# Kernel tuning notes

Hardware: AMD Instinct MI355X
Metric: run time of the kernel (lower is better)

## Reference

```python
import jax, jax.numpy as jnp
import numpy as np

N_UNI = 32; N_G = 4; N_PPG = 8
MAX_D = 100.0; MIN_D = 0.5
SOM_SIGMA = 2.0; G_STD = 2.5
ORIG = jnp.array([-25.6, -25.6, -2.0], jnp.float32); VS = 0.4
NZ = 16; GW = 128; GL = 128; DIM = 128
H_IMG = 352; W_IMG = 1216

def pe(x):
    # positional encoding: num_freqs=6, include_input -> 3 + 36 = 39 dims
    f = 2.0 ** jnp.arange(6, dtype=x.dtype)
    xf = x[..., None] * f  # (...,3,6)
    s = x.shape[:-1]
    return jnp.concatenate([x, jnp.sin(xf).reshape(s + (18,)), jnp.cos(xf).reshape(s + (18,))], axis=-1)

def resnet_fc(z, x, P):
    # pixelNeRF-style ResnetFC with latent injection per block
    w_in, b_in, wz, bz, w0, b0, w1, b1, w_out, b_out = P
    h = x @ w_in + b_in
    for i in range(3):
        h = h + z @ wz[i] + bz[i]
        net = jax.nn.relu(h) @ w0[i] + b0[i]
        h = h + jax.nn.relu(net) @ w1[i] + b1[i]
    return jax.nn.relu(h) @ w_out + b_out

def trilinear(grid, pts):
    # grid: (NZ,GW,GL,DIM); pts: (N,3) lidar coords -> trilinear gather, 0 outside
    g = (pts - ORIG) / VS
    gx, gy, gz = g[:, 0], g[:, 1], g[:, 2]
    inb = (gx >= 0) & (gx <= GW - 1) & (gy >= 0) & (gy <= GL - 1) & (gz >= 0) & (gz <= NZ - 1)
    gx = jnp.clip(gx, 0.0, GW - 1.0); gy = jnp.clip(gy, 0.0, GL - 1.0); gz = jnp.clip(gz, 0.0, NZ - 1.0)
    x0 = jnp.clip(jnp.floor(gx).astype(jnp.int32), 0, GW - 2)
    y0 = jnp.clip(jnp.floor(gy).astype(jnp.int32), 0, GL - 2)
    z0 = jnp.clip(jnp.floor(gz).astype(jnp.int32), 0, NZ - 2)
    fx = gx - x0; fy = gy - y0; fz = gz - z0
    def c(zi, xi, yi, w):
        return grid[zi, xi, yi] * w[:, None]
    feat = (c(z0, x0, y0, (1 - fz) * (1 - fx) * (1 - fy)) + c(z0, x0, y0 + 1, (1 - fz) * (1 - fx) * fy)
            + c(z0, x0 + 1, y0, (1 - fz) * fx * (1 - fy)) + c(z0, x0 + 1, y0 + 1, (1 - fz) * fx * fy)
            + c(z0 + 1, x0, y0, fz * (1 - fx) * (1 - fy)) + c(z0 + 1, x0, y0 + 1, fz * (1 - fx) * fy)
            + c(z0 + 1, x0 + 1, y0, fz * fx * (1 - fy)) + c(z0 + 1, x0 + 1, y0 + 1, fz * fx * fy))
    return feat * inb[:, None].astype(feat.dtype)

def bilinear(img, uv):
    # img: (3,H,W); uv: (N,2) (u=col, v=row) -> (N,3)
    _, H, W = img.shape
    u = jnp.clip(uv[:, 0], 0.0, W - 1.0); v = jnp.clip(uv[:, 1], 0.0, H - 1.0)
    u0 = jnp.clip(jnp.floor(u).astype(jnp.int32), 0, W - 2)
    v0 = jnp.clip(jnp.floor(v).astype(jnp.int32), 0, H - 2)
    fu = u - u0; fv = v - v0
    g = lambda vi, ui: img[:, vi, ui]
    out = (g(v0, u0) * ((1 - fv) * (1 - fu)) + g(v0, u0 + 1) * ((1 - fv) * fu)
           + g(v0 + 1, u0) * (fv * (1 - fu)) + g(v0 + 1, u0 + 1) * (fv * fu))
    return out.T

def _forward(bev_feature, cam_K, img_source, img_target, T_source2infer, T_source2target,
             gaussian_noise, Pm, Pg, sampled_pixels):
    R = sampled_pixels.shape[0]
    # (B, C, W, L) -> (n_z, W, L, dim)
    vf = bev_feature[0].reshape(NZ, DIM, GW, GL).transpose(0, 2, 3, 1)
    inv_K = jnp.linalg.inv(cam_K)
    pix = sampled_pixels.astype(jnp.float32)
    homog = jnp.concatenate([pix, jnp.ones((R, 1), jnp.float32)], axis=1)
    dirs = homog @ inv_K.T
    unit = dirs / jnp.linalg.norm(dirs, axis=1, keepdims=True)  # (R,3) cam frame
    Rsi = T_source2infer[:3, :3]; tsi = T_source2infer[:3, 3]
    viewdir = unit @ Rsi.T  # lidar frame

    # --- predict per-ray gaussian means/stds at coarse segment centers ---
    base = (jnp.arange(N_G, dtype=jnp.float32) + 0.5) * (MAX_D / N_G)
    pg = (unit[:, None, :] * base[None, :, None]).reshape(-1, 3) @ Rsi.T + tsi
    fg = trilinear(vf, pg)
    vdg = jnp.broadcast_to(viewdir[:, None, :], (R, N_G, 3)).reshape(-1, 3)
    og = resnet_fc(fg, jnp.concatenate([pe(pg), vdg], axis=1), Pg)  # (R*N_G,2)
    means = jnp.clip(base[None, :] + og[:, 0].reshape(R, N_G), MIN_D, MAX_D)
    stds = G_STD * jax.nn.sigmoid(og[:, 1].reshape(R, N_G)) + 0.1

    # --- sample points: uniform + gaussian, sorted along ray ---
    d_g = jnp.clip(means[:, :, None] + stds[:, :, None] * gaussian_noise, MIN_D, MAX_D).reshape(R, N_G * N_PPG)
    d_u = jnp.broadcast_to(jnp.linspace(MIN_D, MAX_D, N_UNI, dtype=jnp.float32)[None, :], (R, N_UNI))
    d = jnp.sort(jnp.concatenate([d_u, d_g], axis=1), axis=1)  # (R,64)
    P = d.shape[1]
    pl = (unit[:, None, :] * d[..., None]).reshape(-1, 3) @ Rsi.T + tsi
    fl = trilinear(vf, pl)
    vd = jnp.broadcast_to(viewdir[:, None, :], (R, P, 3)).reshape(-1, 3)
    out = resnet_fc(fl, jnp.concatenate([pe(pl), vd], axis=1), Pm).reshape(R, P, 4)
    sigma = jax.nn.softplus(out[..., 0]); rgb = jax.nn.sigmoid(out[..., 1:])

    # --- volume rendering ---
    deltas = jnp.concatenate([d[:, 1:] - d[:, :-1], jnp.full((R, 1), 1e10, jnp.float32)], axis=1)
    alpha = 1.0 - jnp.exp(-sigma * deltas)
    trans = jnp.cumprod(1.0 - alpha + 1e-10, axis=1)
    trans = jnp.concatenate([jnp.ones((R, 1), jnp.float32), trans[:, :-1]], axis=1)
    w = alpha * trans
    depth = (w * d).sum(axis=1)          # (R,)
    color = (w[..., None] * rgb).sum(axis=1)  # (R,3)

    # --- losses ---
    diff = jnp.abs(means - jax.lax.stop_gradient(depth)[:, None])
    loss_dist = diff.min(axis=1)
    pdf = jnp.exp(-(d[:, None, :] - means[..., None]) ** 2 / (2.0 * stds[..., None] ** 2)) / (stds[..., None] * jnp.sqrt(2.0 * jnp.pi))
    loss_kl = (w * (-jnp.log(pdf.mean(axis=1) + 1e-6))).sum(axis=1)
    src = bilinear(img_source, pix)
    loss_color = jnp.abs(src - color)
    pcam = unit * depth[:, None]
    pt = pcam @ T_source2target[:3, :3].T + T_source2target[:3, 3]
    proj = pt @ cam_K.T
    uv = proj[:, :2] / jnp.clip(proj[:, 2:3], 1e-3)
    tgt = bilinear(img_target, uv)
    loss_reproj = jnp.abs(src - tgt)
    total = loss_reproj.mean() + loss_color.mean() + loss_kl.mean() + 0.01 * loss_dist.mean()
    return total

def setup_inputs() -> dict:
    key = jax.random.key(0)
    def rn(i, shape, s=1.0):
        return jax.random.normal(jax.random.fold_in(key, i), shape, jnp.float32) * s
    R = 4096
    inp = {}
    inp['bev_feature'] = rn(0, (1, NZ * DIM, GW, GL), 0.5)
    inp['cam_K'] = jnp.array([[720.0, 0.0, 608.0], [0.0, 720.0, 176.0], [0.0, 0.0, 1.0]], jnp.float32)
    inp['img_source'] = jax.random.uniform(jax.random.fold_in(key, 1), (3, H_IMG, W_IMG), jnp.float32)
    inp['img_target'] = jax.random.uniform(jax.random.fold_in(key, 2), (3, H_IMG, W_IMG), jnp.float32)
    Rcl = jnp.array([[0.0, 0.0, 1.0], [-1.0, 0.0, 0.0], [0.0, -1.0, 0.0]], jnp.float32)  # cam->lidar axes
    inp['T_source2infer'] = jnp.eye(4, dtype=jnp.float32).at[:3, :3].set(Rcl).at[:3, 3].set(jnp.array([0.5, 0.2, 0.1], jnp.float32))
    inp['T_source2target'] = jnp.eye(4, dtype=jnp.float32).at[0, 3].set(0.8).at[1, 3].set(0.05)
    inp['gaussian_noise'] = rn(3, (R, N_G, N_PPG))
    u = jax.random.randint(jax.random.fold_in(key, 4), (R,), 0, W_IMG)
    v = jax.random.randint(jax.random.fold_in(key, 5), (R,), 0, H_IMG)
    inp['sampled_pixels'] = jnp.stack([u, v], axis=1).astype(jnp.int32)
    for pfx, (i0, d_out) in {'m': (10, 4), 'g': (40, 2)}.items():
        inp[pfx + '_w_in'] = rn(i0, (42, 128), 0.05)
        inp[pfx + '_b_in'] = jnp.zeros((128,), jnp.float32)
        inp[pfx + '_wz'] = rn(i0 + 1, (3, 128, 128), 0.05)
        inp[pfx + '_bz'] = jnp.zeros((3, 128), jnp.float32)
        inp[pfx + '_w0'] = rn(i0 + 2, (3, 128, 128), 0.05)
        inp[pfx + '_b0'] = jnp.zeros((3, 128), jnp.float32)
        inp[pfx + '_w1'] = rn(i0 + 3, (3, 128, 128), 0.05)
        inp[pfx + '_b1'] = jnp.zeros((3, 128), jnp.float32)
        inp[pfx + '_w_out'] = rn(i0 + 4, (128, d_out), 0.05)
        inp[pfx + '_b_out'] = jnp.zeros((d_out,), jnp.float32)
    return inp

def reference(bev_feature, cam_K, img_source, img_target, T_source2infer, T_source2target,
              gaussian_noise, sampled_pixels,
              m_w_in, m_b_in, m_wz, m_bz, m_w0, m_b0, m_w1, m_b1, m_w_out, m_b_out,
              g_w_in, g_b_in, g_wz, g_bz, g_w0, g_b0, g_w1, g_b1, g_w_out, g_b_out):
    Pm = (m_w_in, m_b_in, m_wz, m_bz, m_w0, m_b0, m_w1, m_b1, m_w_out, m_b_out)
    Pg = (g_w_in, g_b_in, g_wz, g_bz, g_w0, g_b0, g_w1, g_b1, g_w_out, g_b_out)
    return _forward(bev_feature, cam_K, img_source, img_target, T_source2infer, T_source2target,
                    gaussian_noise, Pm, Pg, sampled_pixels)
```

## Files before the change

### kernel.cpp

```cpp
#include <hip/hip_runtime.h>

typedef __attribute__((ext_vector_type(8))) short short8;
typedef __attribute__((ext_vector_type(4))) float f32x4;
typedef unsigned short ushort_t;

#define WIMG 1216
#define HIMG 352

__device__ __forceinline__ float sigmoid_(float x){ return 1.f/(1.f+__expf(-x)); }
__device__ __forceinline__ float softplus_(float x){
  return fmaxf(x,0.f) + log1pf(__expf(-fabsf(x)));
}
__device__ __forceinline__ ushort_t f2b(float x){
  union { float f; unsigned u; } v; v.f = x;
  unsigned r = v.u + 0x7FFF + ((v.u >> 16) & 1);
  return (ushort_t)(r >> 16);
}
__device__ __forceinline__ ushort_t f2b_fast(float x){
  union { float f; unsigned u; } v; v.f = x;
  return (ushort_t)((v.u + 0x8000u) >> 16);
}
__device__ __forceinline__ unsigned pack_trunc(float a, float b){
  union { float f; unsigned u; } va, vb; va.f = a; vb.f = b;
  return (va.u >> 16) | (vb.u & 0xFFFF0000u);
}
__device__ __forceinline__ float b2f_lo(unsigned u){
  union { unsigned u; float f; } v; v.u = u << 16; return v.f;
}
__device__ __forceinline__ float b2f_hi(unsigned u){
  union { unsigned u; float f; } v; v.u = u & 0xFFFF0000u; return v.f;
}

__global__ void k_pack(const float* __restrict__ w_in, const float* __restrict__ wz,
                       const float* __restrict__ w0, const float* __restrict__ w1,
                       const float* __restrict__ w_out, int outd,
                       ushort_t* __restrict__ pk){
  int id = blockIdx.x*256 + threadIdx.x;
  if (id >= 39*4096) return;
  int blk = id >> 12;
  int e = id & 4095;
  float val = 0.f;
  if (blk < 38) {
    int nt = e >> 9, lane = (e >> 3) & 63, j = e & 7;
    int kloc = (lane >> 4)*8 + j;
    int n = nt*16 + (lane & 15);
    if (blk < 2) {
      int k = blk*32 + kloc;
      val = (k < 42) ? w_in[k*128 + n] : 0.f;
    } else {
      int g = blk - 2;
      int i = g / 12, r = g % 12, m = r >> 2, ks = r & 3;
      int k = ks*32 + kloc;
      const float* src = (m==0 ? wz : (m==1 ? w0 : w1)) + i*16384;
      val = src[k*128 + n];
    }
  } else if (e < 2048) {
    int ks = e >> 9, lane = (e >> 3) & 63, j = e & 7;
    int k = ks*32 + (lane >> 4)*8 + j;
    int n = lane & 15;
    val = (n < outd) ? w_out[k*outd + n] : 0.f;
  }
  pk[id] = f2b(val);
}

__global__ void k_transpose(const float* __restrict__ src, ushort_t* __restrict__ dst){
  __shared__ float tile[32][33];
  int zx = blockIdx.z;
  int y0 = blockIdx.x * 32;
  int c0 = blockIdx.y * 32;
  int z = zx >> 7, x = zx & 127;
  const float* s = src + (size_t)z*2097152 + (size_t)x*128;
  for (int i = threadIdx.y; i < 32; i += 8)
    tile[i][threadIdx.x] = __builtin_nontemporal_load(s + (size_t)(c0+i)*16384 + (size_t)(y0 + threadIdx.x));
  __syncthreads();
  ushort_t* d = dst + ((size_t)zx*128 + y0)*128 + c0;
  int idx = threadIdx.y*32 + threadIdx.x;
  for (int it = 0; it < 2; ++it) {
    int lin = it*256 + idx;
    int y = lin >> 4, cp = lin & 15;
    unsigned o = pack_trunc(tile[cp*2][y], tile[cp*2+1][y]);
    __builtin_nontemporal_store(o, (unsigned*)(d + (size_t)y*128 + cp*2));
  }
}

__global__ void k_rayinit(const float* __restrict__ camK, const int* __restrict__ pix,
                          const float* __restrict__ Tsi,
                          float* __restrict__ unit, float* __restrict__ viewdir, int R){
  int r = blockIdx.x*blockDim.x + threadIdx.x;
  if (r >= R) return;
  float a=camK[0],b=camK[1],c=camK[2],d=camK[3],e=camK[4],f=camK[5],g=camK[6],h=camK[7],i=camK[8];
  float c00 = e*i-f*h, c01 = c*h-b*i, c02 = b*f-c*e;
  float c10 = f*g-d*i, c11 = a*i-c*g, c12 = c*d-a*f;
  float c20 = d*h-e*g, c21 = b*g-a*h, c22 = a*e-b*d;
  float det = a*c00 + b*c10 + c*c20;
  float id = 1.f/det;
  float u = (float)pix[2*r], v = (float)pix[2*r+1];
  float dx = (c00*u + c01*v + c02)*id;
  float dy = (c10*u + c11*v + c12)*id;
  float dz = (c20*u + c21*v + c22)*id;
  float n = sqrtf(dx*dx+dy*dy+dz*dz);
  dx/=n; dy/=n; dz/=n;
  unit[3*r]=dx; unit[3*r+1]=dy; unit[3*r+2]=dz;
  viewdir[3*r]   = Tsi[0]*dx + Tsi[1]*dy + Tsi[2]*dz;
  viewdir[3*r+1] = Tsi[4]*dx + Tsi[5]*dy + Tsi[6]*dz;
  viewdir[3*r+2] = Tsi[8]*dx + Tsi[9]*dy + Tsi[10]*dz;
}

template<int KS>
__device__ __forceinline__ void gemm_accT(const ushort_t* lds, int pitch,
                                          const ushort_t* __restrict__ pkW,
                                          f32x4 acc[2][4], int wave, int lane)
{
  int l15 = lane & 15, quad = lane >> 4;
  short8 w[KS][2];
  #pragma unroll
  for (int ks = 0; ks < KS; ++ks)
    #pragma unroll
    for (int ct = 0; ct < 2; ++ct)
      w[ks][ct] = *(const short8*)(pkW + (size_t)((ks*8 + wave*2 + ct)*64 + lane)*8);
  #pragma unroll
  for (int ks = 0; ks < KS; ++ks) {
    short8 b[4];
    #pragma unroll
    for (int nt = 0; nt < 4; ++nt)
      b[nt] = *(const short8*)(lds + (nt*16 + l15)*pitch + ks*32 + quad*8);
    #pragma unroll
    for (int ct = 0; ct < 2; ++ct)
      #pragma unroll
      for (int nt = 0; nt < 4; ++nt)
        acc[ct][nt] = __builtin_amdgcn_mfma_f32_16x16x32_bf16(w[ks][ct], b[nt], acc[ct][nt], 0,0,0);
  }
}

__device__ __forceinline__ void store_reluT(ushort_t* buf, const f32x4 acc[2][4], int wave, int lane){
  int l15 = lane & 15, quad = lane >> 4;
  #pragma unroll
  for (int ct = 0; ct < 2; ++ct)
    #pragma unroll
    for (int nt = 0; nt < 4; ++nt) {
      float r0 = fmaxf(acc[ct][nt][0], 0.f);
      float r1 = fmaxf(acc[ct][nt][1], 0.f);
      float r2 = fmaxf(acc[ct][nt][2], 0.f);
      float r3 = fmaxf(acc[ct][nt][3], 0.f);
      uint2 o; o.x = pack_trunc(r0, r1); o.y = pack_trunc(r2, r3);
      *(uint2*)(buf + (nt*16 + l15)*136 + (wave*2+ct)*16 + quad*4) = o;
    }
}

template<int OUTD, int RAY_SHIFT>
__global__ __launch_bounds__(256, 4)
void k_fused(const ushort_t* __restrict__ vfh, const float* __restrict__ vf0, int mode,
             const float* __restrict__ unit, const float* __restrict__ viewdir,
             const float* __restrict__ Tsi, const float* __restrict__ dvals,
             const ushort_t* __restrict__ pk,
             const float* __restrict__ b_in, const float* __restrict__ bzv,
             const float* __restrict__ b0v, const float* __restrict__ b1v,
             const float* __restrict__ b_out,
             float* __restrict__ means, float* __restrict__ stds, float* __restrict__ outbuf)
{
  __shared__ int   sOff[64];
  __shared__ float sW[64][8];
  __shared__ float sPx[64], sPy[64], sPz[64], sVx[64], sVy[64], sVz[64];
  __shared__ ushort_t zf[64*136];
  __shared__ ushort_t Wb[64*136];

  int tid = threadIdx.x;
  int qbase = blockIdx.x * 64;

  if (tid < 64) {
    int q = qbase + tid;
    int ray = q >> RAY_SHIFT;
    float t;
    if constexpr (OUTD == 2) t = ((float)(q & 3) + 0.5f) * 25.f;
    else                     t = dvals[q];
    float ux = unit[3*ray], uy = unit[3*ray+1], uz = unit[3*ray+2];
    float wx=ux*t, wy=uy*t, wz=uz*t;
    float px = Tsi[0]*wx + Tsi[1]*wy + Tsi[2]*wz + Tsi[3];
    float py = Tsi[4]*wx + Tsi[5]*wy + Tsi[6]*wz + Tsi[7];
    float pz = Tsi[8]*wx + Tsi[9]*wy + Tsi[10]*wz + Tsi[11];
    sPx[tid]=px; sPy[tid]=py; sPz[tid]=pz;
    sVx[tid]=viewdir[3*ray]; sVy[tid]=viewdir[3*ray+1]; sVz[tid]=viewdir[3*ray+2];
    float gx = (px + 25.6f)*2.5f;
    float gy = (py + 25.6f)*2.5f;
    float gz = (pz + 2.0f)*2.5f;
    bool inb = (gx>=0.f)&&(gx<=127.f)&&(gy>=0.f)&&(gy<=127.f)&&(gz>=0.f)&&(gz<=15.f);
    gx = fminf(fmaxf(gx,0.f),127.f);
    gy = fminf(fmaxf(gy,0.f),127.f);
    gz = fminf(fmaxf(gz,0.f),15.f);
    int x0 = min(max((int)floorf(gx),0),126);
    int y0 = min(max((int)floorf(gy),0),126);
    int z0 = min(max((int)floorf(gz),0),14);
    float fx = gx-(float)x0, fy = gy-(float)y0, fz = gz-(float)z0;
    float sc = inb ? 1.f : 0.f;
    float ax0 = 1.f-fx, ay0 = 1.f-fy;
    float az0 = (1.f-fz)*sc, az1 = fz*sc;
    float q00 = ax0*ay0, q01 = ax0*fy, q10 = fx*ay0, q11 = fx*fy;
    sW[tid][0] = az0*q00; sW[tid][1] = az0*q01; sW[tid][2] = az0*q10; sW[tid][3] = az0*q11;
    sW[tid][4] = az1*q00; sW[tid][5] = az1*q01; sW[tid][6] = az1*q10; sW[tid][7] = az1*q11;
    sOff[tid] = mode ? (((z0*128 + x0)*128 + y0)*128)
                     : (z0*2097152 + x0*128 + y0);
  }
  __syncthreads();

  for (int it = 0; it < 4; ++it) {
    int lin = it*256 + tid;
    int p = lin >> 4, cb = lin & 15;
    float4 wA = *(const float4*)&sW[p][0];
    float4 wB = *(const float4*)&sW[p][4];
    float r0=0,r1=0,r2=0,r3=0,r4=0,r5=0,r6=0,r7=0;
    if (mode) {
      const ushort_t* b = vfh + sOff[p] + cb*8;
      uint4 v;
      #define ACC8(PTR, W) \
        v = *(const uint4*)(PTR); \
        r0 += (W)*b2f_lo(v.x); r1 += (W)*b2f_hi(v.x); \
        r2 += (W)*b2f_lo(v.y); r3 += (W)*b2f_hi(v.y); \
        r4 += (W)*b2f_lo(v.z); r5 += (W)*b2f_hi(v.z); \
        r6 += (W)*b2f_lo(v.w); r7 += (W)*b2f_hi(v.w);
      ACC8(b,                     wA.x)
      ACC8(b + 128,               wA.y)
      ACC8(b + 16384,             wA.z)
      ACC8(b + 16384 + 128,       wA.w)
      ACC8(b + 2097152,           wB.x)
      ACC8(b + 2097152 + 128,     wB.y)
      ACC8(b + 2097152 + 16384,   wB.z)
      ACC8(b + 2097152 + 16512,   wB.w)
      #undef ACC8
    } else {
      const float* bsrc = vf0 + sOff[p];
      float rr[8];
      #pragma unroll
      for (int k = 0; k < 8; ++k) {
        const float* bc = bsrc + (size_t)(cb*8 + k)*16384;
        rr[k] = wA.x*bc[0] + wA.y*bc[1] + wA.z*bc[128] + wA.w*bc[129]
              + wB.x*bc[2097152] + wB.y*bc[2097153] + wB.z*bc[2097280] + wB.w*bc[2097281];
      }
      r0=rr[0]; r1=rr[1]; r2=rr[2]; r3=rr[3]; r4=rr[4]; r5=rr[5]; r6=rr[6]; r7=rr[7];
    }
    uint4 o;
    o.x = pack_trunc(r0, r1); o.y = pack_trunc(r2, r3);
    o.z = pack_trunc(r4, r5); o.w = pack_trunc(r6, r7);
    *(uint4*)(zf + p*136 + cb*8) = o;
  }

  for (int it = 0; it < 16; ++it) {
    int lin = it*256 + tid;
    int p = lin >> 6, d = lin & 63;
    float val = 0.f;
    if (d < 3)      val = (d==0)?sPx[p]:((d==1)?sPy[p]:sPz[p]);
    else if (d < 39) {
      int s = d - 3; bool isSin = (s < 18); if (!isSin) s -= 18;
      int axis = s/6, fi = s%6;
      float base = (axis==0)?sPx[p]:((axis==1)?sPy[p]:sPz[p]);
      float arg = base * (float)(1 << fi);
      val = isSin ? __sinf(arg) : __cosf(arg);
    } else if (d < 42) {
      val = (d==39)?sVx[p]:((d==40)?sVy[p]:sVz[p]);
    }
    Wb[p*72 + d] = f2b_fast(val);
  }
  __syncthreads();

  int wave = tid >> 6, lane = tid & 63;
  int l15 = lane & 15, quad = lane >> 4;
  int cbase = wave*32 + quad*4;

  f32x4 h[2][4];
  {
    f32x4 bi0 = *(const f32x4*)(b_in + cbase);
    f32x4 bi1 = *(const f32x4*)(b_in + cbase + 16);
    #pragma unroll
    for (int nt = 0; nt < 4; ++nt) { h[0][nt] = bi0; h[1][nt] = bi1; }
  }
  gemm_accT<2>(Wb, 72, pk, h, wave, lane);

  const ushort_t* pkl = pk + 2*4096;
  #pragma unroll 1
  for (int i = 0; i < 3; ++i) {
    gemm_accT<4>(zf, 136, pkl + (size_t)(i*12)*4096, h, wave, lane);
    {
      f32x4 bz0 = *(const f32x4*)(bzv + i*128 + cbase);
      f32x4 bz1 = *(const f32x4*)(bzv + i*128 + cbase + 16);
      #pragma unroll
      for (int nt = 0; nt < 4; ++nt) { h[0][nt] += bz0; h[1][nt] += bz1; }
    }
    __syncthreads();
    store_reluT(Wb, h, wave, lane);
    __syncthreads();
    f32x4 net[2][4];
    {
      f32x4 c0b = *(const f32x4*)(b0v + i*128 + cbase);
      f32x4 c1b = *(const f32x4*)(b0v + i*128 + cbase + 16);
      #pragma unroll
      for (int nt = 0; nt < 4; ++nt) { net[0][nt] = c0b; net[1][nt] = c1b; }
    }
    gemm_accT<4>(Wb, 136, pkl + (size_t)(i*12+4)*4096, net, wave, lane);
    __syncthreads();
    store_reluT(Wb, net, wave, lane);
    __syncthreads();
    gemm_accT<4>(Wb, 136, pkl + (size_t)(i*12+8)*4096, h, wave, lane);
    {
      f32x4 o0b = *(const f32x4*)(b1v + i*128 + cbase);
      f32x4 o1b = *(const f32x4*)(b1v + i*128 + cbase + 16);
      #pragma unroll
      for (int nt = 0; nt < 4; ++nt) { h[0][nt] += o0b; h[1][nt] += o1b; }
    }
  }
  __syncthreads();
  store_reluT(Wb, h, wave, lane);
  __syncthreads();

  {
    const ushort_t* pkw = pk + 38*4096;
    f32x4 oa = (f32x4){0.f,0.f,0.f,0.f};
    #pragma unroll
    for (int ks = 0; ks < 4; ++ks) {
      short8 w = *(const short8*)(pkw + (size_t)(ks*64 + lane)*8);
      short8 b = *(const short8*)(Wb + (wave*16 + l15)*136 + ks*32 + quad*8);
      oa = __builtin_amdgcn_mfma_f32_16x16x32_bf16(w, b, oa, 0,0,0);
    }
    if (quad == 0) {
      int q = qbase + wave*16 + l15;
      if constexpr (OUTD == 4) {
        float4 o = { oa[0] + b_out[0], oa[1] + b_out[1], oa[2] + b_out[2], oa[3] + b_out[3] };
        *(float4*)(outbuf + (size_t)q*4) = o;
      } else {
        int g = q & 3;
        means[q] = fminf(fmaxf(((float)g + 0.5f)*25.f + oa[0] + b_out[0], 0.5f), 100.f);
        stds[q]  = 2.5f*sigmoid_(oa[1] + b_out[1]) + 0.1f;
      }
    }
  }
}

__global__ void k_sortd(const float* __restrict__ means, const float* __restrict__ stds,
                        const float* __restrict__ noise, float* __restrict__ dsort, int R){
  __shared__ float buf[4][64];
  int lr = threadIdx.x >> 6, p = threadIdx.x & 63;
  int ray = blockIdx.x*4 + lr;
  float val;
  if (p < 32) val = 0.5f + (float)p * (99.5f/31.f);
  else {
    int idx = p - 32, g = idx >> 3, s = idx & 7;
    float mu = means[ray*4+g], sd = stds[ray*4+g];
    val = fminf(fmaxf(mu + sd*noise[(ray*4+g)*8 + s], 0.5f), 100.f);
  }
  buf[lr][p] = val;
  __syncthreads();
  int rank = 0;
  for (int k = 0; k < 64; ++k) {
    float o = buf[lr][k];
    rank += (o < val) || (o == val && k < p);
  }
  dsort[ray*64 + rank] = val;
}

__device__ __forceinline__ void bilin3(const float* __restrict__ img, float u, float v, float* out){
  u = fminf(fmaxf(u, 0.f), (float)(WIMG-1));
  v = fminf(fmaxf(v, 0.f), (float)(HIMG-1));
  int u0 = min(max((int)floorf(u),0), WIMG-2);
  int v0 = min(max((int)floorf(v),0), HIMG-2);
  float fu = u - (float)u0, fv = v - (float)v0;
  float w00=(1.f-fv)*(1.f-fu), w01=(1.f-fv)*fu, w10=fv*(1.f-fu), w11=fv*fu;
  #pragma unroll
  for (int c = 0; c < 3; ++c) {
    const float* b = img + (size_t)c*(HIMG*WIMG) + (size_t)v0*WIMG + u0;
    out[c] = w00*b[0] + w01*b[1] + w10*b[WIMG] + w11*b[WIMG+1];
  }
}

__global__ void k_render(const float* __restrict__ outbuf, const float* __restrict__ dsort,
                         const float* __restrict__ means, const float* __restrict__ stds,
                         const float* __restrict__ unit,
                         const float* __restrict__ img_src, const float* __restrict__ img_tgt,
                         const int* __restrict__ pix, const float* __restrict__ camK,
                         const float* __restrict__ Tst, float* __restrict__ rayloss, int R){
  int gid = blockIdx.x*blockDim.x + threadIdx.x;
  int r = gid >> 6, lane = gid & 63;
  if (r >= R) return;
  float d = dsort[(size_t)r*64 + lane];
  float dn = __shfl_down(d, 1);
  float delta = (lane < 63) ? (dn - d) : 1e10f;
  float4 o = *(const float4*)(outbuf + (size_t)r*256 + lane*4);
  float sig = softplus_(o.x);
  float alpha = 1.f - __expf(-sig*delta);
  float om = 1.f - alpha + 1e-10f;
  float prod = om;
  #pragma unroll
  for (int off = 1; off < 64; off <<= 1) {
    float v = __shfl_up(prod, off);
    if (lane >= off) prod *= v;
  }
  float texc = __shfl_up(prod, 1);
  if (lane == 0) texc = 1.f;
  float w = alpha * texc;
  float m0=means[r*4],m1=means[r*4+1],m2=means[r*4+2],m3=means[r*4+3];
  float s0=stds[r*4], s1=stds[r*4+1], s2=stds[r*4+2], s3=stds[r*4+3];
  float t0=(d-m0)/s0, t1=(d-m1)/s1, t2=(d-m2)/s2, t3=(d-m3)/s3;
  float pm = 0.25f*0.3989422804014327f*(__expf(-0.5f*t0*t0)/s0 + __expf(-0.5f*t1*t1)/s1
                                      + __expf(-0.5f*t2*t2)/s2 + __expf(-0.5f*t3*t3)/s3);
  float kl  = w * (-__logf(pm + 1e-6f));
  float dep = w * d;
  float c0 = w * sigmoid_(o.y);
  float c1 = w * sigmoid_(o.z);
  float c2 = w * sigmoid_(o.w);
  #pragma unroll
  for (int off = 32; off; off >>= 1) {
    dep += __shfl_xor(dep, off);
    c0  += __shfl_xor(c0, off);
    c1  += __shfl_xor(c1, off);
    c2  += __shfl_xor(c2, off);
    kl  += __shfl_xor(kl, off);
  }
  if (lane == 0) {
    float ld = fminf(fminf(fabsf(m0-dep),fabsf(m1-dep)), fminf(fabsf(m2-dep),fabsf(m3-dep)));
    float src[3], tgt[3];
    float u = (float)pix[2*r], v = (float)pix[2*r+1];
    bilin3(img_src, u, v, src);
    float ux=unit[3*r],uy=unit[3*r+1],uz=unit[3*r+2];
    float pcx=ux*dep, pcy=uy*dep, pcz=uz*dep;
    float ptx = Tst[0]*pcx + Tst[1]*pcy + Tst[2]*pcz + Tst[3];
    float pty = Tst[4]*pcx + Tst[5]*pcy + Tst[6]*pcz + Tst[7];
    float ptz = Tst[8]*pcx + Tst[9]*pcy + Tst[10]*pcz + Tst[11];
    float prx = camK[0]*ptx + camK[1]*pty + camK[2]*ptz;
    float pry = camK[3]*ptx + camK[4]*pty + camK[5]*ptz;
    float prz = camK[6]*ptx + camK[7]*pty + camK[8]*ptz;
    prz = fmaxf(prz, 0.001f);
    bilin3(img_tgt, prx/prz, pry/prz, tgt);
    float lrepr = fabsf(src[0]-tgt[0])+fabsf(src[1]-tgt[1])+fabsf(src[2]-tgt[2]);
    float lcol  = fabsf(src[0]-c0)+fabsf(src[1]-c1)+fabsf(src[2]-c2);
    float invR = 1.f/(float)R;
    rayloss[r] = (lrepr + lcol) * (invR/3.f) + kl*invR + 0.01f*ld*invR;
  }
}

__global__ void k_reduce(const float* __restrict__ rayloss, float* __restrict__ out, int R){
  __shared__ float sm[256];
  float acc = 0.f;
  for (int i = threadIdx.x; i < R; i += 256) acc += rayloss[i];
  sm[threadIdx.x] = acc;
  __syncthreads();
  for (int s = 128; s > 0; s >>= 1) {
    if ((int)threadIdx.x < s) sm[threadIdx.x] += sm[threadIdx.x + s];
    __syncthreads();
  }
  if (threadIdx.x == 0) out[0] = sm[0];
}

extern "C" void kernel_launch(void* const* d_in, const int* in_sizes, int n_in,
                              void* d_out, int out_size, void* d_ws, size_t ws_size,
                              hipStream_t stream)
{
  const float* bev   = (const float*)d_in[0];
  const float* camK  = (const float*)d_in[1];
  const float* img_s = (const float*)d_in[2];
  const float* img_t = (const float*)d_in[3];
  const float* Tsi   = (const float*)d_in[4];
  const float* Tst   = (const float*)d_in[5];
  const float* noise = (const float*)d_in[6];
  const int*   pix   = (const int*)d_in[7];
  const float* m_w_in=(const float*)d_in[8];  const float* m_b_in=(const float*)d_in[9];
  const float* m_wz  =(const float*)d_in[10]; const float* m_bz  =(const float*)d_in[11];
  const float* m_w0  =(const float*)d_in[12]; const float* m_b0  =(const float*)d_in[13];
  const float* m_w1  =(const float*)d_in[14]; const float* m_b1  =(const float*)d_in[15];
  const float* m_wo  =(const float*)d_in[16]; const float* m_bo  =(const float*)d_in[17];
  const float* g_w_in=(const float*)d_in[18]; const float* g_b_in=(const float*)d_in[19];
  const float* g_wz  =(const float*)d_in[20]; const float* g_bz  =(const float*)d_in[21];
  const float* g_w0  =(const float*)d_in[22]; const float* g_b0  =(const float*)d_in[23];
  const float* g_w1  =(const float*)d_in[24]; const float* g_b1  =(const float*)d_in[25];
  const float* g_wo  =(const float*)d_in[26]; const float* g_bo  =(const float*)d_in[27];

  int R = in_sizes[7] / 2;
  float* ws = (float*)d_ws;
  size_t off = 0;
  float* unitb = ws + off; off += (size_t)R*3;
  float* vdirb = ws + off; off += (size_t)R*3;
  float* means = ws + off; off += (size_t)R*4;
  float* stds  = ws + off; off += (size_t)R*4;
  float* dsort = ws + off; off += (size_t)R*64;
  float* outbf = ws + off; off += (size_t)R*256;
  float* rlos  = ws + off; off += (size_t)R;
  ushort_t* pkM = (ushort_t*)(ws + off);
  ushort_t* pkG = pkM + 39*4096;
  off += 39*4096 + 64;
  off = (off + 63) & ~(size_t)63;
  ushort_t* vfh = (ushort_t*)(ws + off);
  size_t need = off*4ull + (size_t)16*128*128*128*2ull;
  int mode = (ws_size >= need) ? 1 : 0;

  k_pack<<<624,256,0,stream>>>(m_w_in, m_wz, m_w0, m_w1, m_wo, 4, pkM);
  k_pack<<<624,256,0,stream>>>(g_w_in, g_wz, g_w0, g_w1, g_wo, 2, pkG);
  if (mode) {
    dim3 g(4,4,2048), b(32,8);
    k_transpose<<<g,b,0,stream>>>(bev, vfh);
  }
  k_rayinit<<<(R+255)/256,256,0,stream>>>(camK,pix,Tsi,unitb,vdirb,R);
  k_fused<2,2><<<R/16,256,0,stream>>>(vfh,bev,mode,unitb,vdirb,Tsi,nullptr,pkG,
      g_b_in,g_bz,g_b0,g_b1,g_bo, means,stds,nullptr);
  k_sortd<<<R/4,256,0,stream>>>(means,stds,noise,dsort,R);
  k_fused<4,6><<<R,256,0,stream>>>(vfh,bev,mode,unitb,vdirb,Tsi,dsort,pkM,
      m_b_in,m_bz,m_b0,m_b1,m_bo, nullptr,nullptr,outbf);
  k_render<<<R/4,256,0,stream>>>(outbf,dsort,means,stds,unitb,img_s,img_t,pix,camK,Tst,rlos,R);
  k_reduce<<<1,256,0,stream>>>(rlos,(float*)d_out,R);
}
```

Measured before the change: 458.8 us.

## Fuse ray init, depth sort and loss reduction into neighbouring kernels; retile MLP fragments

Ray-direction setup moves into the guide-MLP kernel, and the per-ray depth sampling and sort move into its epilogue. The final loss reduction becomes a per-block atomicAdd in the render kernel, and the output is zeroed inside the pack kernel. Together these remove three launches and their intermediate buffers. The MLP GEMM switches to a pre-swizzled fragment LDS layout with a 2x2 wave split, and the BEV transpose uses 64x64 tiles with vectorized loads and stores. The atomic accumulation makes the loss sum order nondeterministic.

```diff
diff --git a/kernel.cpp b/kernel.cpp
--- a/kernel.cpp
+++ b/kernel.cpp
@@ -2,6 +2,7 @@
 
 typedef __attribute__((ext_vector_type(8))) short short8;
 typedef __attribute__((ext_vector_type(4))) float f32x4;
+typedef __attribute__((ext_vector_type(2))) unsigned u32x2;
 typedef unsigned short ushort_t;
 
 #define WIMG 1216
@@ -34,7 +35,8 @@
 __global__ void k_pack(const float* __restrict__ w_in, const float* __restrict__ wz,
                        const float* __restrict__ w0, const float* __restrict__ w1,
                        const float* __restrict__ w_out, int outd,
-                       ushort_t* __restrict__ pk){
+                       ushort_t* __restrict__ pk, float* __restrict__ out0){
+  if (out0 && blockIdx.x == 0 && threadIdx.x == 0) out0[0] = 0.f;
   int id = blockIdx.x*256 + threadIdx.x;
   if (id >= 39*4096) return;
   int blk = id >> 12;
@@ -63,95 +65,79 @@
   pk[id] = f2b(val);
 }
 
-__global__ void k_transpose(const float* __restrict__ src, ushort_t* __restrict__ dst){
-  __shared__ float tile[32][33];
+__global__ __launch_bounds__(256) void k_transpose(const float* __restrict__ src, ushort_t* __restrict__ dst){
+  __shared__ float tile[64][65];
   int zx = blockIdx.z;
-  int y0 = blockIdx.x * 32;
-  int c0 = blockIdx.y * 32;
+  int y0 = blockIdx.x * 64;
+  int c0 = blockIdx.y * 64;
   int z = zx >> 7, x = zx & 127;
-  const float* s = src + (size_t)z*2097152 + (size_t)x*128;
-  for (int i = threadIdx.y; i < 32; i += 8)
-    tile[i][threadIdx.x] = __builtin_nontemporal_load(s + (size_t)(c0+i)*16384 + (size_t)(y0 + threadIdx.x));
+  const float* s = src + (size_t)z*2097152 + (size_t)c0*16384 + (size_t)x*128 + y0;
+  int tid = threadIdx.x;
+  int r0 = tid >> 4, f4 = tid & 15;
+  #pragma unroll
+  for (int it = 0; it < 4; ++it) {
+    int c = it*16 + r0;
+    f32x4 v = __builtin_nontemporal_load((const f32x4*)(s + (size_t)c*16384 + f4*4));
+    tile[c][f4*4+0]=v.x; tile[c][f4*4+1]=v.y; tile[c][f4*4+2]=v.z; tile[c][f4*4+3]=v.w;
+  }
   __syncthreads();
   ushort_t* d = dst + ((size_t)zx*128 + y0)*128 + c0;
-  int idx = threadIdx.y*32 + threadIdx.x;
-  for (int it = 0; it < 2; ++it) {
-    int lin = it*256 + idx;
-    int y = lin >> 4, cp = lin & 15;
-    unsigned o = pack_trunc(tile[cp*2][y], tile[cp*2+1][y]);
-    __builtin_nontemporal_store(o, (unsigned*)(d + (size_t)y*128 + cp*2));
-  }
-}
-
-__global__ void k_rayinit(const float* __restrict__ camK, const int* __restrict__ pix,
-                          const float* __restrict__ Tsi,
-                          float* __restrict__ unit, float* __restrict__ viewdir, int R){
-  int r = blockIdx.x*blockDim.x + threadIdx.x;
-  if (r >= R) return;
-  float a=camK[0],b=camK[1],c=camK[2],d=camK[3],e=camK[4],f=camK[5],g=camK[6],h=camK[7],i=camK[8];
-  float c00 = e*i-f*h, c01 = c*h-b*i, c02 = b*f-c*e;
-  float c10 = f*g-d*i, c11 = a*i-c*g, c12 = c*d-a*f;
-  float c20 = d*h-e*g, c21 = b*g-a*h, c22 = a*e-b*d;
-  float det = a*c00 + b*c10 + c*c20;
-  float id = 1.f/det;
-  float u = (float)pix[2*r], v = (float)pix[2*r+1];
-  float dx = (c00*u + c01*v + c02)*id;
-  float dy = (c10*u + c11*v + c12)*id;
-  float dz = (c20*u + c21*v + c22)*id;
-  float n = sqrtf(dx*dx+dy*dy+dz*dz);
-  dx/=n; dy/=n; dz/=n;
-  unit[3*r]=dx; unit[3*r+1]=dy; unit[3*r+2]=dz;
-  viewdir[3*r]   = Tsi[0]*dx + Tsi[1]*dy + Tsi[2]*dz;
-  viewdir[3*r+1] = Tsi[4]*dx + Tsi[5]*dy + Tsi[6]*dz;
-  viewdir[3*r+2] = Tsi[8]*dx + Tsi[9]*dy + Tsi[10]*dz;
+  #pragma unroll
+  for (int it = 0; it < 4; ++it) {
+    int y = it*16 + r0;
+    float a0 = tile[f4*4+0][y], a1 = tile[f4*4+1][y];
+    float a2 = tile[f4*4+2][y], a3 = tile[f4*4+3][y];
+    u32x2 o; o.x = pack_trunc(a0,a1); o.y = pack_trunc(a2,a3);
+    __builtin_nontemporal_store(o, (u32x2*)(d + (size_t)y*128 + f4*4));
+  }
 }
 
 template<int KS>
-__device__ __forceinline__ void gemm_accT(const ushort_t* lds, int pitch,
+__device__ __forceinline__ void gemm_frag(const ushort_t* lds,
                                           const ushort_t* __restrict__ pkW,
-                                          f32x4 acc[2][4], int wave, int lane)
+                                          f32x4 acc[4][2], int chalf, int phalf, int lane)
 {
+  #pragma unroll
+  for (int ks = 0; ks < KS; ++ks) {
+    short8 b[2];
+    #pragma unroll
+    for (int ntL = 0; ntL < 2; ++ntL)
+      b[ntL] = *(const short8*)(lds + (ks*4 + phalf*2 + ntL)*512 + lane*8);
+    #pragma unroll
+    for (int i = 0; i < 4; ++i) {
+      short8 w = *(const short8*)(pkW + (size_t)((ks*8 + chalf*4 + i)*64 + lane)*8);
+      #pragma unroll
+      for (int ntL = 0; ntL < 2; ++ntL)
+        acc[i][ntL] = __builtin_amdgcn_mfma_f32_16x16x32_bf16(w, b[ntL], acc[i][ntL], 0,0,0);
+    }
+  }
+}
+
+__device__ __forceinline__ void store_reluF(ushort_t* buf, const f32x4 acc[4][2],
+                                            int chalf, int phalf, int lane){
   int l15 = lane & 15, quad = lane >> 4;
-  short8 w[KS][2];
-  #pragma unroll
-  for (int ks = 0; ks < KS; ++ks)
-    #pragma unroll
-    for (int ct = 0; ct < 2; ++ct)
-      w[ks][ct] = *(const short8*)(pkW + (size_t)((ks*8 + wave*2 + ct)*64 + lane)*8);
-  #pragma unroll
-  for (int ks = 0; ks < KS; ++ks) {
-    short8 b[4];
-    #pragma unroll
-    for (int nt = 0; nt < 4; ++nt)
-      b[nt] = *(const short8*)(lds + (nt*16 + l15)*pitch + ks*32 + quad*8);
-    #pragma unroll
-    for (int ct = 0; ct < 2; ++ct)
-      #pragma unroll
-      for (int nt = 0; nt < 4; ++nt)
-        acc[ct][nt] = __builtin_amdgcn_mfma_f32_16x16x32_bf16(w[ks][ct], b[nt], acc[ct][nt], 0,0,0);
-  }
-}
-
-__device__ __forceinline__ void store_reluT(ushort_t* buf, const f32x4 acc[2][4], int wave, int lane){
-  int l15 = lane & 15, quad = lane >> 4;
-  #pragma unroll
-  for (int ct = 0; ct < 2; ++ct)
-    #pragma unroll
-    for (int nt = 0; nt < 4; ++nt) {
-      float r0 = fmaxf(acc[ct][nt][0], 0.f);
-      float r1 = fmaxf(acc[ct][nt][1], 0.f);
-      float r2 = fmaxf(acc[ct][nt][2], 0.f);
-      float r3 = fmaxf(acc[ct][nt][3], 0.f);
-      uint2 o; o.x = pack_trunc(r0, r1); o.y = pack_trunc(r2, r3);
-      *(uint2*)(buf + (nt*16 + l15)*136 + (wave*2+ct)*16 + quad*4) = o;
-    }
-}
-
-template<int OUTD, int RAY_SHIFT>
+  #pragma unroll
+  for (int i = 0; i < 4; ++i) {
+    int c = chalf*64 + i*16 + quad*4;
+    int ksp = c >> 5, k3 = (c >> 3) & 3, jj = c & 7;
+    #pragma unroll
+    for (int ntL = 0; ntL < 2; ++ntL) {
+      int nt = phalf*2 + ntL;
+      uint2 o;
+      o.x = pack_trunc(fmaxf(acc[i][ntL][0],0.f), fmaxf(acc[i][ntL][1],0.f));
+      o.y = pack_trunc(fmaxf(acc[i][ntL][2],0.f), fmaxf(acc[i][ntL][3],0.f));
+      *(uint2*)(buf + (ksp*4 + nt)*512 + (k3*16 + l15)*8 + jj) = o;
+    }
+  }
+}
+
+template<int OUTD>
 __global__ __launch_bounds__(256, 4)
 void k_fused(const ushort_t* __restrict__ vfh, const float* __restrict__ vf0, int mode,
-             const float* __restrict__ unit, const float* __restrict__ viewdir,
-             const float* __restrict__ Tsi, const float* __restrict__ dvals,
+             const float* __restrict__ camK, const int* __restrict__ pix,
+             const float* __restrict__ noise,
+             float* __restrict__ unit, float* __restrict__ viewdir,
+             const float* __restrict__ Tsi, float* __restrict__ dsort,
              const ushort_t* __restrict__ pk,
              const float* __restrict__ b_in, const float* __restrict__ bzv,
              const float* __restrict__ b0v, const float* __restrict__ b1v,
@@ -160,26 +146,62 @@
 {
   __shared__ int   sOff[64];
   __shared__ float sW[64][8];
-  __shared__ float sPx[64], sPy[64], sPz[64], sVx[64], sVy[64], sVz[64];
-  __shared__ ushort_t zf[64*136];
-  __shared__ ushort_t Wb[64*136];
+  __shared__ float sPx[64], sPy[64], sPz[64];
+  __shared__ float sUx[16], sUy[16], sUz[16], sVx[16], sVy[16], sVz[16];
+  __shared__ float sMean[64], sStd[64];
+  __shared__ __align__(16) ushort_t zf[16*512];
+  __shared__ __align__(16) ushort_t Wb[16*512];
 
   int tid = threadIdx.x;
   int qbase = blockIdx.x * 64;
 
+  if constexpr (OUTD == 2) {
+    if (tid < 16) {
+      int gray = (qbase >> 2) + tid;
+      float a=camK[0],b=camK[1],c=camK[2],d=camK[3],e=camK[4],f=camK[5],g=camK[6],h=camK[7],i=camK[8];
+      float c00 = e*i-f*h, c01 = c*h-b*i, c02 = b*f-c*e;
+      float c10 = f*g-d*i, c11 = a*i-c*g, c12 = c*d-a*f;
+      float c20 = d*h-e*g, c21 = b*g-a*h, c22 = a*e-b*d;
+      float det = a*c00 + b*c10 + c*c20;
+      float id = 1.f/det;
+      float u = (float)pix[2*gray], v = (float)pix[2*gray+1];
+      float dx = (c00*u + c01*v + c02)*id;
+      float dy = (c10*u + c11*v + c12)*id;
+      float dz = (c20*u + c21*v + c22)*id;
+      float n = sqrtf(dx*dx+dy*dy+dz*dz);
+      dx/=n; dy/=n; dz/=n;
+      sUx[tid]=dx; sUy[tid]=dy; sUz[tid]=dz;
+      unit[3*gray]=dx; unit[3*gray+1]=dy; unit[3*gray+2]=dz;
+      float vx = Tsi[0]*dx + Tsi[1]*dy + Tsi[2]*dz;
+      float vy = Tsi[4]*dx + Tsi[5]*dy + Tsi[6]*dz;
+      float vz = Tsi[8]*dx + Tsi[9]*dy + Tsi[10]*dz;
+      sVx[tid]=vx; sVy[tid]=vy; sVz[tid]=vz;
+      viewdir[3*gray]=vx; viewdir[3*gray+1]=vy; viewdir[3*gray+2]=vz;
+    }
+  } else {
+    if (tid == 0) {
+      int ray = blockIdx.x;
+      sUx[0]=unit[3*ray]; sUy[0]=unit[3*ray+1]; sUz[0]=unit[3*ray+2];
+      sVx[0]=viewdir[3*ray]; sVy[0]=viewdir[3*ray+1]; sVz[0]=viewdir[3*ray+2];
+    }
+  }
+  __syncthreads();
+
   if (tid < 64) {
-    int q = qbase + tid;
-    int ray = q >> RAY_SHIFT;
-    float t;
-    if constexpr (OUTD == 2) t = ((float)(q & 3) + 0.5f) * 25.f;
-    else                     t = dvals[q];
-    float ux = unit[3*ray], uy = unit[3*ray+1], uz = unit[3*ray+2];
+    float t, ux, uy, uz;
+    if constexpr (OUTD == 2) {
+      t = ((float)(tid & 3) + 0.5f) * 25.f;
+      int lr = tid >> 2;
+      ux = sUx[lr]; uy = sUy[lr]; uz = sUz[lr];
+    } else {
+      t = dsort[qbase + tid];
+      ux = sUx[0]; uy = sUy[0]; uz = sUz[0];
+    }
     float wx=ux*t, wy=uy*t, wz=uz*t;
     float px = Tsi[0]*wx + Tsi[1]*wy + Tsi[2]*wz + Tsi[3];
     float py = Tsi[4]*wx + Tsi[5]*wy + Tsi[6]*wz + Tsi[7];
     float pz = Tsi[8]*wx + Tsi[9]*wy + Tsi[10]*wz + Tsi[11];
     sPx[tid]=px; sPy[tid]=py; sPz[tid]=pz;
-    sVx[tid]=viewdir[3*ray]; sVy[tid]=viewdir[3*ray+1]; sVz[tid]=viewdir[3*ray+2];
     float gx = (px + 25.6f)*2.5f;
     float gy = (py + 25.6f)*2.5f;
     float gz = (pz + 2.0f)*2.5f;
@@ -240,74 +262,80 @@
     uint4 o;
     o.x = pack_trunc(r0, r1); o.y = pack_trunc(r2, r3);
     o.z = pack_trunc(r4, r5); o.w = pack_trunc(r6, r7);
-    *(uint4*)(zf + p*136 + cb*8) = o;
-  }
-
-  for (int it = 0; it < 16; ++it) {
-    int lin = it*256 + tid;
-    int p = lin >> 6, d = lin & 63;
-    float val = 0.f;
-    if (d < 3)      val = (d==0)?sPx[p]:((d==1)?sPy[p]:sPz[p]);
-    else if (d < 39) {
-      int s = d - 3; bool isSin = (s < 18); if (!isSin) s -= 18;
-      int axis = s/6, fi = s%6;
-      float base = (axis==0)?sPx[p]:((axis==1)?sPy[p]:sPz[p]);
-      float arg = base * (float)(1 << fi);
-      val = isSin ? __sinf(arg) : __cosf(arg);
-    } else if (d < 42) {
-      val = (d==39)?sVx[p]:((d==40)?sVy[p]:sVz[p]);
-    }
-    Wb[p*72 + d] = f2b_fast(val);
+    int T = (cb >> 2)*4 + (p >> 4);
+    int lanep = (cb & 3)*16 + (p & 15);
+    *(uint4*)(zf + T*512 + lanep*8) = o;
+  }
+
+  {
+    int p = tid & 63, dg = tid >> 6;
+    float px = sPx[p], py = sPy[p], pz = sPz[p];
+    int lr = (OUTD == 2) ? (p >> 2) : 0;
+    float vx = sVx[lr], vy = sVy[lr], vz = sVz[lr];
+    #pragma unroll 1
+    for (int it = 0; it < 16; ++it) {
+      int d = it*4 + dg;
+      float val = 0.f;
+      if (d < 3)      val = (d==0)?px:((d==1)?py:pz);
+      else if (d < 39) {
+        int s = d - 3; bool isSin = (s < 18); if (!isSin) s -= 18;
+        int axis = s/6, fi = s%6;
+        float base = (axis==0)?px:((axis==1)?py:pz);
+        float arg = base * (float)(1 << fi);
+        val = isSin ? __sinf(arg) : __cosf(arg);
+      } else if (d < 42) {
+        val = (d==39)?vx:((d==40)?vy:vz);
+      }
+      int addr = (d>>5)*2048 + (p>>4)*512 + (((d>>3)&3)*16 + (p&15))*8 + (d&7);
+      Wb[addr] = f2b_fast(val);
+    }
   }
   __syncthreads();
 
   int wave = tid >> 6, lane = tid & 63;
   int l15 = lane & 15, quad = lane >> 4;
-  int cbase = wave*32 + quad*4;
-
-  f32x4 h[2][4];
-  {
-    f32x4 bi0 = *(const f32x4*)(b_in + cbase);
-    f32x4 bi1 = *(const f32x4*)(b_in + cbase + 16);
-    #pragma unroll
-    for (int nt = 0; nt < 4; ++nt) { h[0][nt] = bi0; h[1][nt] = bi1; }
-  }
-  gemm_accT<2>(Wb, 72, pk, h, wave, lane);
+  int chalf = wave >> 1, phalf = wave & 1;
+  int cbase = chalf*64 + quad*4;
+
+  f32x4 h[4][2];
+  #pragma unroll
+  for (int i = 0; i < 4; ++i) {
+    f32x4 bi = *(const f32x4*)(b_in + cbase + i*16);
+    h[i][0] = bi; h[i][1] = bi;
+  }
+  gemm_frag<2>(Wb, pk, h, chalf, phalf, lane);
 
   const ushort_t* pkl = pk + 2*4096;
   #pragma unroll 1
-  for (int i = 0; i < 3; ++i) {
-    gemm_accT<4>(zf, 136, pkl + (size_t)(i*12)*4096, h, wave, lane);
-    {
-      f32x4 bz0 = *(const f32x4*)(bzv + i*128 + cbase);
-      f32x4 bz1 = *(const f32x4*)(bzv + i*128 + cbase + 16);
-      #pragma unroll
-      for (int nt = 0; nt < 4; ++nt) { h[0][nt] += bz0; h[1][nt] += bz1; }
+  for (int i3 = 0; i3 < 3; ++i3) {
+    gemm_frag<4>(zf, pkl + (size_t)(i3*12)*4096, h, chalf, phalf, lane);
+    #pragma unroll
+    for (int i = 0; i < 4; ++i) {
+      f32x4 bz = *(const f32x4*)(bzv + i3*128 + cbase + i*16);
+      h[i][0] += bz; h[i][1] += bz;
     }
     __syncthreads();
-    store_reluT(Wb, h, wave, lane);
+    store_reluF(Wb, h, chalf, phalf, lane);
     __syncthreads();
-    f32x4 net[2][4];
-    {
-      f32x4 c0b = *(const f32x4*)(b0v + i*128 + cbase);
-      f32x4 c1b = *(const f32x4*)(b0v + i*128 + cbase + 16);
-      #pragma unroll
-      for (int nt = 0; nt < 4; ++nt) { net[0][nt] = c0b; net[1][nt] = c1b; }
-    }
-    gemm_accT<4>(Wb, 136, pkl + (size_t)(i*12+4)*4096, net, wave, lane);
+    f32x4 net[4][2];
+    #pragma unroll
+    for (int i = 0; i < 4; ++i) {
+      f32x4 c0b = *(const f32x4*)(b0v + i3*128 + cbase + i*16);
+      net[i][0] = c0b; net[i][1] = c0b;
+    }
+    gemm_frag<4>(Wb, pkl + (size_t)(i3*12+4)*4096, net, chalf, phalf, lane);
     __syncthreads();
-    store_reluT(Wb, net, wave, lane);
+    store_reluF(Wb, net, chalf, phalf, lane);
     __syncthreads();
-    gemm_accT<4>(Wb, 136, pkl + (size_t)(i*12+8)*4096, h, wave, lane);
-    {
-      f32x4 o0b = *(const f32x4*)(b1v + i*128 + cbase);
-      f32x4 o1b = *(const f32x4*)(b1v + i*128 + cbase + 16);
-      #pragma unroll
-      for (int nt = 0; nt < 4; ++nt) { h[0][nt] += o0b; h[1][nt] += o1b; }
-    }
-  }
-  __syncthreads();
-  store_reluT(Wb, h, wave, lane);
+    gemm_frag<4>(Wb, pkl + (size_t)(i3*12+8)*4096, h, chalf, phalf, lane);
+    #pragma unroll
+    for (int i = 0; i < 4; ++i) {
+      f32x4 o1b = *(const f32x4*)(b1v + i3*128 + cbase + i*16);
+      h[i][0] += o1b; h[i][1] += o1b;
+    }
+  }
+  __syncthreads();
+  store_reluF(Wb, h, chalf, phalf, lane);
   __syncthreads();
 
   {
@@ -316,43 +344,58 @@
     #pragma unroll
     for (int ks = 0; ks < 4; ++ks) {
       short8 w = *(const short8*)(pkw + (size_t)(ks*64 + lane)*8);
-      short8 b = *(const short8*)(Wb + (wave*16 + l15)*136 + ks*32 + quad*8);
+      short8 b = *(const short8*)(Wb + (ks*4 + wave)*512 + lane*8);
       oa = __builtin_amdgcn_mfma_f32_16x16x32_bf16(w, b, oa, 0,0,0);
     }
     if (quad == 0) {
-      int q = qbase + wave*16 + l15;
+      int lq = wave*16 + l15;
+      int q = qbase + lq;
       if constexpr (OUTD == 4) {
         float4 o = { oa[0] + b_out[0], oa[1] + b_out[1], oa[2] + b_out[2], oa[3] + b_out[3] };
         *(float4*)(outbuf + (size_t)q*4) = o;
       } else {
         int g = q & 3;
-        means[q] = fminf(fmaxf(((float)g + 0.5f)*25.f + oa[0] + b_out[0], 0.5f), 100.f);
-        stds[q]  = 2.5f*sigmoid_(oa[1] + b_out[1]) + 0.1f;
+        float m = fminf(fmaxf(((float)g + 0.5f)*25.f + oa[0] + b_out[0], 0.5f), 100.f);
+        float sd = 2.5f*sigmoid_(oa[1] + b_out[1]) + 0.1f;
+        means[q] = m; stds[q] = sd;
+        sMean[lq] = m; sStd[lq] = sd;
       }
     }
   }
-}
-
-__global__ void k_sortd(const float* __restrict__ means, const float* __restrict__ stds,
-                        const float* __restrict__ noise, float* __restrict__ dsort, int R){
-  __shared__ float buf[4][64];
-  int lr = threadIdx.x >> 6, p = threadIdx.x & 63;
-  int ray = blockIdx.x*4 + lr;
-  float val;
-  if (p < 32) val = 0.5f + (float)p * (99.5f/31.f);
-  else {
-    int idx = p - 32, g = idx >> 3, s = idx & 7;
-    float mu = means[ray*4+g], sd = stds[ray*4+g];
-    val = fminf(fmaxf(mu + sd*noise[(ray*4+g)*8 + s], 0.5f), 100.f);
-  }
-  buf[lr][p] = val;
-  __syncthreads();
-  int rank = 0;
-  for (int k = 0; k < 64; ++k) {
-    float o = buf[lr][k];
-    rank += (o < val) || (o == val && k < p);
-  }
-  dsort[ray*64 + rank] = val;
+
+  if constexpr (OUTD == 2) {
+    __syncthreads();
+    float* fbuf = (float*)zf;
+    int lr = tid >> 4;
+    int sbase = (tid & 15) * 4;
+    float vals[4];
+    #pragma unroll
+    for (int t = 0; t < 4; ++t) {
+      int slot = sbase + t;
+      float val;
+      if (slot < 32) val = 0.5f + (float)slot * (99.5f/31.f);
+      else {
+        int idx = slot - 32, g = idx >> 3, s = idx & 7;
+        int lq = lr*4 + g;
+        float mu = sMean[lq], sd = sStd[lq];
+        val = fminf(fmaxf(mu + sd*noise[(size_t)(qbase + lq)*8 + s], 0.5f), 100.f);
+      }
+      fbuf[lr*64 + slot] = val;
+      vals[t] = val;
+    }
+    __syncthreads();
+    int rk[4] = {0,0,0,0};
+    for (int k = 0; k < 64; ++k) {
+      float o = fbuf[lr*64 + k];
+      #pragma unroll
+      for (int t = 0; t < 4; ++t)
+        rk[t] += (o < vals[t]) || (o == vals[t] && k < sbase + t);
+    }
+    int gray = (qbase >> 2) + lr;
+    #pragma unroll
+    for (int t = 0; t < 4; ++t)
+      dsort[(size_t)gray*64 + rk[t]] = vals[t];
+  }
 }
 
 __device__ __forceinline__ void bilin3(const float* __restrict__ img, float u, float v, float* out){
@@ -374,10 +417,10 @@
                          const float* __restrict__ unit,
                          const float* __restrict__ img_src, const float* __restrict__ img_tgt,
                          const int* __restrict__ pix, const float* __restrict__ camK,
-                         const float* __restrict__ Tst, float* __restrict__ rayloss, int R){
+                         const float* __restrict__ Tst, float* __restrict__ loss_out, int R){
+  __shared__ float accw[4];
   int gid = blockIdx.x*blockDim.x + threadIdx.x;
   int r = gid >> 6, lane = gid & 63;
-  if (r >= R) return;
   float d = dsort[(size_t)r*64 + lane];
   float dn = __shfl_down(d, 1);
   float delta = (lane < 63) ? (dn - d) : 1e10f;
@@ -430,21 +473,11 @@
     float lrepr = fabsf(src[0]-tgt[0])+fabsf(src[1]-tgt[1])+fabsf(src[2]-tgt[2]);
     float lcol  = fabsf(src[0]-c0)+fabsf(src[1]-c1)+fabsf(src[2]-c2);
     float invR = 1.f/(float)R;
-    rayloss[r] = (lrepr + lcol) * (invR/3.f) + kl*invR + 0.01f*ld*invR;
-  }
-}
-
-__global__ void k_reduce(const float* __restrict__ rayloss, float* __restrict__ out, int R){
-  __shared__ float sm[256];
-  float acc = 0.f;
-  for (int i = threadIdx.x; i < R; i += 256) acc += rayloss[i];
-  sm[threadIdx.x] = acc;
-  __syncthreads();
-  for (int s = 128; s > 0; s >>= 1) {
-    if ((int)threadIdx.x < s) sm[threadIdx.x] += sm[threadIdx.x + s];
-    __syncthreads();
-  }
-  if (threadIdx.x == 0) out[0] = sm[0];
+    accw[threadIdx.x >> 6] = (lrepr + lcol) * (invR/3.f) + kl*invR + 0.01f*ld*invR;
+  }
+  __syncthreads();
+  if (threadIdx.x == 0)
+    atomicAdd(loss_out, accw[0]+accw[1]+accw[2]+accw[3]);
 }
 
 extern "C" void kernel_launch(void* const* d_in, const int* in_sizes, int n_in,
@@ -479,7 +512,6 @@
   float* stds  = ws + off; off += (size_t)R*4;
   float* dsort = ws + off; off += (size_t)R*64;
   float* outbf = ws + off; off += (size_t)R*256;
-  float* rlos  = ws + off; off += (size_t)R;
   ushort_t* pkM = (ushort_t*)(ws + off);
   ushort_t* pkG = pkM + 39*4096;
   off += 39*4096 + 64;
@@ -488,18 +520,16 @@
   size_t need = off*4ull + (size_t)16*128*128*128*2ull;
   int mode = (ws_size >= need) ? 1 : 0;
 
-  k_pack<<<624,256,0,stream>>>(m_w_in, m_wz, m_w0, m_w1, m_wo, 4, pkM);
-  k_pack<<<624,256,0,stream>>>(g_w_in, g_wz, g_w0, g_w1, g_wo, 2, pkG);
+  k_pack<<<624,256,0,stream>>>(m_w_in, m_wz, m_w0, m_w1, m_wo, 4, pkM, (float*)d_out);
+  k_pack<<<624,256,0,stream>>>(g_w_in, g_wz, g_w0, g_w1, g_wo, 2, pkG, nullptr);
   if (mode) {
-    dim3 g(4,4,2048), b(32,8);
-    k_transpose<<<g,b,0,stream>>>(bev, vfh);
-  }
-  k_rayinit<<<(R+255)/256,256,0,stream>>>(camK,pix,Tsi,unitb,vdirb,R);
-  k_fused<2,2><<<R/16,256,0,stream>>>(vfh,bev,mode,unitb,vdirb,Tsi,nullptr,pkG,
+    dim3 g(2,2,2048);
+    k_transpose<<<g,256,0,stream>>>(bev, vfh);
+  }
+  k_fused<2><<<R/16,256,0,stream>>>(vfh,bev,mode,camK,pix,noise,unitb,vdirb,Tsi,dsort,pkG,
       g_b_in,g_bz,g_b0,g_b1,g_bo, means,stds,nullptr);
-  k_sortd<<<R/4,256,0,stream>>>(means,stds,noise,dsort,R);
-  k_fused<4,6><<<R,256,0,stream>>>(vfh,bev,mode,unitb,vdirb,Tsi,dsort,pkM,
-      m_b_in,m_bz,m_b0,m_b1,m_bo, nullptr,nullptr,outbf);
-  k_render<<<R/4,256,0,stream>>>(outbf,dsort,means,stds,unitb,img_s,img_t,pix,camK,Tst,rlos,R);
-  k_reduce<<<1,256,0,stream>>>(rlos,(float*)d_out,R);
-}
+  k_fused<4><<<R,256,0,stream>>>(vfh,bev,mode,camK,pix,noise,unitb,vdirb,Tsi,dsort,pkM,
+      m_b_in,m_bz,m_b0,m_b1,m_bo, means,stds,outbf);
+  k_render<<<R/4,256,0,stream>>>(outbf,dsort,means,stds,unitb,img_s,img_t,pix,camK,Tst,
+                                 (float*)d_out,R);
+}
```

After: 530.9 us. 15.7% more time.
